# Kernel tuning notes

Measured on AMD Instinct MI355X. Metric: run time of the kernel, lower is better.

Reference implementation:

```python
import jax, jax.numpy as jnp
import numpy as np

D = 512
H = 8
W = 128  # window_size
HD = D // H
EPS = 1e-5


def _layernorm(x, g, b):
    mu = jnp.mean(x, axis=-1, keepdims=True)
    var = jnp.mean(jnp.square(x - mu), axis=-1, keepdims=True)
    return (x - mu) * jax.lax.rsqrt(var + EPS) * g + b


def setup_inputs() -> dict:
    key = jax.random.key(0)
    ks = jax.random.split(key, 6)
    B, S = 4, 8192
    src = jax.random.normal(ks[0], (B, S, D), jnp.float32)
    sc = 1.0 / np.sqrt(D)
    in_proj_w = jax.random.normal(ks[1], (3 * D, D), jnp.float32) * sc
    in_proj_b = jnp.zeros((3 * D,), jnp.float32)
    out_w = jax.random.normal(ks[2], (D, D), jnp.float32) * sc
    out_b = jnp.zeros((D,), jnp.float32)
    w1 = jax.random.normal(ks[3], (4 * D, D), jnp.float32) * sc
    b1 = jnp.zeros((4 * D,), jnp.float32)
    w2 = jax.random.normal(ks[4], (D, 4 * D), jnp.float32) * (1.0 / np.sqrt(4 * D))
    b2 = jnp.zeros((D,), jnp.float32)
    return {
        'src': src,
        'in_proj_w': in_proj_w, 'in_proj_b': in_proj_b,
        'out_w': out_w, 'out_b': out_b,
        'ln1_g': jnp.ones((D,), jnp.float32), 'ln1_b': jnp.zeros((D,), jnp.float32),
        'w1': w1, 'b1': b1, 'w2': w2, 'b2': b2,
        'ln2_g': jnp.ones((D,), jnp.float32), 'ln2_b': jnp.zeros((D,), jnp.float32),
    }


def reference(src, in_proj_w, in_proj_b, out_w, out_b, ln1_g, ln1_b,
              w1, b1, w2, b2, ln2_g, ln2_b):
    B, S, _ = src.shape
    nW = S // W
    x = src.reshape(B, nW, W, D)  # block-diagonal windows
    # packed qkv projection (torch MultiheadAttention in_proj)
    qkv = jnp.einsum('bnwd,ed->bnwe', x, in_proj_w) + in_proj_b
    q, k, v = jnp.split(qkv, 3, axis=-1)
    q = q.reshape(B, nW, W, H, HD)
    k = k.reshape(B, nW, W, H, HD)
    v = v.reshape(B, nW, W, H, HD)
    scores = jnp.einsum('bnqhd,bnkhd->bnhqk', q, k) / np.sqrt(HD)
    probs = jax.nn.softmax(scores, axis=-1)
    attn = jnp.einsum('bnhqk,bnkhd->bnqhd', probs, v).reshape(B, nW, W, D)
    attn = jnp.einsum('bnwd,ed->bnwe', attn, out_w) + out_b
    x = _layernorm(x + attn, ln1_g, ln1_b)
    ff = jnp.einsum('bnwf,df->bnwd', jax.nn.relu(jnp.einsum('bnwd,fd->bnwf', x, w1) + b1), w2) + b2
    x = _layernorm(x + ff, ln2_g, ln2_b)
    return x.reshape(B, S, D)
```

## Files before the change

### kernel.cpp

```cpp
#include <hip/hip_runtime.h>
#include <hip/hip_bf16.h>
#include <math.h>

typedef __bf16 bf16;
typedef bf16 bf16x8 __attribute__((ext_vector_type(8)));
typedef bf16 bf16x4 __attribute__((ext_vector_type(4)));
typedef float f32x4 __attribute__((ext_vector_type(4)));

#define MFMA16(a, b, c) __builtin_amdgcn_mfma_f32_16x16x32_bf16(a, b, c, 0, 0, 0)

__device__ __forceinline__ uint32_t swz(uint32_t base, uint32_t row, uint32_t rs, uint32_t cb) {
    return base + row * rs + (((cb >> 4) ^ (row & 7u)) << 4) + (cb & 15u);
}

__device__ __forceinline__ void gload16(const void* g, void* l) {
    __builtin_amdgcn_global_load_lds((const __attribute__((address_space(1))) void*)g,
                                     (__attribute__((address_space(3))) void*)l, 16, 0, 0);
}



__global__ void wcvt_kernel(const float* __restrict__ wqkv, const float* __restrict__ wout,
                            const float* __restrict__ w1f, const float* __restrict__ w2f,
                            bf16* __restrict__ o) {
    int i = blockIdx.x * blockDim.x + threadIdx.x;
    const float* s;
    int soff, doff;
    if (i < 98304) {
        int u = i;
        int tile = u >> 10, c = (u >> 8) & 3, nn = u & 255;
        int n = (tile >> 4) * 256 + nn;
        int k = (tile & 15) * 32 + c * 8;
        s = wqkv; soff = n * 512 + k; doff = u * 8;
    } else if (i < 131072) {
        int u = i - 98304;
        int tile = u >> 11, c = (u >> 9) & 3, nn = u & 511;
        int k = tile * 32 + c * 8;
        s = wout; soff = nn * 512 + k; doff = 786432 + u * 8;
    } else if (i < 262144) {
        int u = i - 131072;
        int tile = u >> 10, c = (u >> 8) & 3, nn = u & 255;
        int n = (tile >> 4) * 256 + nn;
        int k = (tile & 15) * 32 + c * 8;
        s = w1f; soff = n * 512 + k; doff = 1048576 + u * 8;
    } else {
        int u = i - 262144;
        int t = u >> 11, c = (u >> 9) & 3, nn = u & 511;
        int k = t * 32 + c * 8;
        s = w2f; soff = nn * 2048 + k; doff = 2097152 + u * 8;
    }
    float4 v0 = *(const float4*)(s + soff);
    float4 v1 = *(const float4*)(s + soff + 4);
    bf16x8 h = { (bf16)v0.x, (bf16)v0.y, (bf16)v0.z, (bf16)v0.w,
                 (bf16)v1.x, (bf16)v1.y, (bf16)v1.z, (bf16)v1.w };
    *(bf16x8*)(o + doff) = h;
}

__global__ void xcvt_kernel(float* __restrict__ src) {
    int row = blockIdx.x * 4 + (threadIdx.x >> 6);
    int l = threadIdx.x & 63;
    float* rp = src + (size_t)row * 512 + l * 8;
    float4 v0 = *(const float4*)rp;
    float4 v1 = *(const float4*)(rp + 4);
    asm volatile("s_waitcnt vmcnt(0)" ::: "memory");
    bf16x8 h = { (bf16)v0.x, (bf16)v0.y, (bf16)v0.z, (bf16)v0.w,
                 (bf16)v1.x, (bf16)v1.y, (bf16)v1.z, (bf16)v1.w };
    *(bf16x8*)((bf16*)(src + (size_t)row * 512) + l * 8) = h;
}

#define N256_LOOP(NT)                                                                  \
    int ib = 0;                                                                        \
    _Pragma("unroll 1")                                                                \
    for (int t = 0; t < (NT); ++t) {                                                   \
        int in2 = ib + 2; if (in2 >= 3) in2 -= 3;                                      \
        const uint32_t A0 = (uint32_t)ib * 8192u;                                      \
        const uint32_t B0 = 24576u + (uint32_t)ib * 16384u;                            \
        bf16x8 a[4], b[4];                                                             \
        _Pragma("unroll")                                                              \
        for (int i = 0; i < 4; ++i)                                                    \
            a[i] = *(const bf16x8*)(smem + A0 + quad * 2048 + (wm * 64 + i * 16 + l16) * 16); \
        _Pragma("unroll")                                                              \
        for (int nt = 0; nt < 4; ++nt)                                                 \
            b[nt] = *(const bf16x8*)(smem + B0 + quad * 4096 + (wn * 64 + nt * 16 + l16) * 16); \
        if (t + 2 < (NT)) { STAGE_A(in2, t + 2); STAGE_B2(in2, t + 2, 0); STAGE_B2(in2, t + 2, 1); } \
        _Pragma("unroll")                                                              \
        for (int nt = 0; nt < 4; ++nt)                                                 \
            _Pragma("unroll")                                                          \
            for (int i = 0; i < 4; ++i) acc[i][nt] = MFMA16(a[i], b[nt], acc[i][nt]);  \
        if (t + 2 < (NT)) asm volatile("s_waitcnt vmcnt(3)" ::: "memory");             \
        else              asm volatile("s_waitcnt vmcnt(0)" ::: "memory");             \
        __builtin_amdgcn_s_barrier();                                                  \
        ib = (ib == 2) ? 0 : ib + 1;                                                   \
    }

#define PHASED_LOOP(NT)                                                                \
    int ib = 0;                                                                        \
    _Pragma("unroll 1")                                                                \
    for (int t = 0; t < (NT); ++t) {                                                   \
        int in2 = ib + 2; if (in2 >= 3) in2 -= 3;                                      \
        const uint32_t A0 = (uint32_t)ib * 8192u;                                      \
        const uint32_t B0 = 24576u + (uint32_t)ib * 32768u;                            \
        bf16x8 a[4], b[8];                                                             \
                                                                \
        _Pragma("unroll")                                                              \
        for (int i = 0; i < 4; ++i)                                                    \
            a[i] = *(const bf16x8*)(smem + A0 + quad * 2048 + (wm * 64 + i * 16 + l16) * 16); \
        _Pragma("unroll")                                                              \
        for (int nt = 0; nt < 4; ++nt)                                                 \
            b[nt] = *(const bf16x8*)(smem + B0 + quad * 8192 + (wn * 128 + nt * 16 + l16) * 16); \
        if (t + 2 < (NT)) { STAGE_A(in2, t + 2); STAGE_B(in2, t + 2, 0); }             \
        __builtin_amdgcn_s_barrier();                                                  \
        asm volatile("s_waitcnt lgkmcnt(0)" ::: "memory");                             \
        __builtin_amdgcn_sched_barrier(0);                                             \
        __builtin_amdgcn_s_setprio(1);                                                 \
        _Pragma("unroll")                                                              \
        for (int nt = 0; nt < 4; ++nt)                                                 \
            _Pragma("unroll")                                                          \
            for (int i = 0; i < 4; ++i) acc[i][nt] = MFMA16(a[i], b[nt], acc[i][nt]);  \
        __builtin_amdgcn_s_setprio(0);                                                 \
        __builtin_amdgcn_s_barrier();                                                  \
                                                                \
        _Pragma("unroll")                                                              \
        for (int nt = 4; nt < 8; ++nt)                                                 \
            b[nt] = *(const bf16x8*)(smem + B0 + quad * 8192 + (wn * 128 + nt * 16 + l16) * 16); \
        if (t + 2 < (NT)) { STAGE_B(in2, t + 2, 1); STAGE_B(in2, t + 2, 2); STAGE_B(in2, t + 2, 3); } \
        __builtin_amdgcn_s_barrier();                                                  \
        asm volatile("s_waitcnt lgkmcnt(0)" ::: "memory");                             \
        __builtin_amdgcn_sched_barrier(0);                                             \
        __builtin_amdgcn_s_setprio(1);                                                 \
        _Pragma("unroll")                                                              \
        for (int nt = 4; nt < 8; ++nt)                                                 \
            _Pragma("unroll")                                                          \
            for (int i = 0; i < 4; ++i) acc[i][nt] = MFMA16(a[i], b[nt], acc[i][nt]);  \
        __builtin_amdgcn_s_setprio(0);                                                 \
        if (t + 2 < (NT)) asm volatile("s_waitcnt vmcnt(5)" ::: "memory");             \
        else              asm volatile("s_waitcnt vmcnt(0)" ::: "memory");             \
        __builtin_amdgcn_s_barrier();                                                  \
        ib = (ib == 2) ? 0 : ib + 1;                                                   \
    }

extern "C" __global__ __launch_bounds__(512, 4)
void qkv_kernel(const char* __restrict__ xb, const char* __restrict__ Wqkvp,
                const float* __restrict__ bqkv, char* __restrict__ qOb,
                char* __restrict__ kvb) {
    extern __shared__ char smem[];
    const int tid = threadIdx.x;
    const int w = tid >> 6, lane = tid & 63, l16 = lane & 15, quad = lane >> 4;
    const int wm = w >> 2, wn = w & 3;
    const int mb = blockIdx.x, cb = blockIdx.y;

    f32x4 acc[4][4];
#pragma unroll
    for (int i = 0; i < 4; ++i)
#pragma unroll
        for (int nt = 0; nt < 4; ++nt) acc[i][nt] = (f32x4){0.f, 0.f, 0.f, 0.f};

#define STAGE_A(ib_, t_)                                                               \
    {                                                                                  \
        int ca = w >> 1, rg = w & 1;                                                   \
        gload16(xb + (size_t)(mb * 128 + rg * 64 + lane) * 2048 + (t_) * 64 + ca * 16, \
                smem + (uint32_t)(ib_) * 8192u + ca * 2048 + rg * 1024);               \
    }
#define STAGE_B2(ib_, t_, j_)                                                          \
    {                                                                                  \
        int idx = w * 2 + (j_), c = idx >> 2, ng = idx & 3;                            \
        gload16(Wqkvp + (size_t)(cb * 16 + (t_)) * 16384 + c * 4096 + ng * 1024 + lane * 16, \
                smem + 24576u + (uint32_t)(ib_) * 16384u + (uint32_t)c * 4096 + (uint32_t)ng * 1024); \
    }

    STAGE_A(0, 0); STAGE_B2(0, 0, 0); STAGE_B2(0, 0, 1);
    STAGE_A(1, 1); STAGE_B2(1, 1, 0); STAGE_B2(1, 1, 1);
    asm volatile("s_waitcnt vmcnt(3)" ::: "memory");
    __builtin_amdgcn_s_barrier();

    N256_LOOP(16)
#undef STAGE_A
#undef STAGE_B2

    const uint32_t sb = 24576u + (uint32_t)w * 2048u;
#pragma unroll
    for (int i = 0; i < 4; ++i) {
#pragma unroll
        for (int nt = 0; nt < 4; ++nt) {
            float bb = bqkv[cb * 256 + wn * 64 + nt * 16 + l16];
#pragma unroll
            for (int r = 0; r < 4; ++r)
                *(bf16*)(smem + swz(sb, quad * 4 + r, 128, (nt * 16 + l16) * 2)) =
                    (bf16)(acc[i][nt][r] + bb);
        }
        asm volatile("s_waitcnt lgkmcnt(0)" ::: "memory");
#pragma unroll
        for (int t2 = 0; t2 < 2; ++t2) {
            int row = t2 * 8 + (lane >> 3), ch = lane & 7;
            bf16x8 v = *(bf16x8*)(smem + swz(sb, row, 128, ch * 16));
            size_t row_g = (size_t)(mb * 128 + wm * 64 + i * 16 + row);
            int cbyte = wn * 128 + ch * 16;
            if (cb < 2)      *(bf16x8*)(qOb + row_g * 1024 + cb * 512 + cbyte) = v;
            else if (cb < 4) *(bf16x8*)(kvb + row_g * 2048 + (cb - 2) * 512 + cbyte) = v;
            else             *(bf16x8*)(kvb + row_g * 2048 + 1024 + (cb - 4) * 512 + cbyte) = v;
        }
        asm volatile("s_waitcnt lgkmcnt(0)" ::: "memory");
    }
}

#define AVT 0u
#define ASCR 16384u
extern "C" __global__ __launch_bounds__(512, 4)
void attn_kernel(char* __restrict__ qOb, const char* __restrict__ kvb) {
    extern __shared__ char smem[];
    const int tid = threadIdx.x;
    const int wid = tid >> 6, lane = tid & 63, l16 = lane & 15, quad = lane >> 4;
    const int win = blockIdx.x >> 3, head = blockIdx.x & 7;
    const size_t wrow0 = (size_t)win * 128;
    f32x4 zero4 = { 0.f, 0.f, 0.f, 0.f };

    {
        int key = tid >> 2, d0 = (tid & 3) * 16;
        const char* vs = kvb + (wrow0 + key) * 2048 + 1024 + head * 128 + d0 * 2;
#pragma unroll
        for (int j = 0; j < 2; ++j) {
            bf16x8 v = *(const bf16x8*)(vs + j * 16);
#pragma unroll
            for (int e = 0; e < 8; ++e)
                *(bf16*)(smem + swz(AVT, d0 + j * 8 + e, 256, key * 2)) = v[e];
        }
    }
    __syncthreads();

    bf16x8 qf[2];
#pragma unroll
    for (int ks = 0; ks < 2; ++ks)
        qf[ks] = *(const bf16x8*)(qOb + (wrow0 + wid * 16 + l16) * 1024 + head * 128 + ks * 64 + quad * 16);

    f32x4 sa[8];
#pragma unroll
    for (int nt = 0; nt < 8; ++nt) sa[nt] = zero4;
#pragma unroll
    for (int nt = 0; nt < 8; ++nt)
#pragma unroll
        for (int ks = 0; ks < 2; ++ks) {
            bf16x8 kb = *(const bf16x8*)(kvb + (wrow0 + nt * 16 + l16) * 2048 + head * 128 + ks * 64 + quad * 16);
            sa[nt] = MFMA16(qf[ks], kb, sa[nt]);
        }
#pragma unroll
    for (int nt = 0; nt < 8; ++nt) sa[nt] *= 0.125f;
#pragma unroll
    for (int r = 0; r < 4; ++r) {
        float m = sa[0][r];
#pragma unroll
        for (int nt = 1; nt < 8; ++nt) m = fmaxf(m, sa[nt][r]);
#pragma unroll
        for (int sft = 1; sft < 16; sft <<= 1) m = fmaxf(m, __shfl_xor(m, sft, 64));
        float s = 0.f;
#pragma unroll
        for (int nt = 0; nt < 8; ++nt) {
            float e = __expf(sa[nt][r] - m);
            sa[nt][r] = e;
            s += e;
        }
#pragma unroll
        for (int sft = 1; sft < 16; sft <<= 1) s += __shfl_xor(s, sft, 64);
        float inv = 1.0f / s;
#pragma unroll
        for (int nt = 0; nt < 8; ++nt) sa[nt][r] *= inv;
    }

    const uint32_t sb = ASCR + (uint32_t)wid * 2048;
    bf16x8 pf[4];
#pragma unroll
    for (int hf = 0; hf < 2; ++hf) {
#pragma unroll
        for (int nt = 0; nt < 4; ++nt)
#pragma unroll
            for (int r = 0; r < 4; ++r)
                *(bf16*)(smem + swz(sb, quad * 4 + r, 128, (nt * 16 + l16) * 2)) = (bf16)sa[hf * 4 + nt][r];
        asm volatile("s_waitcnt lgkmcnt(0)" ::: "memory");
#pragma unroll
        for (int ks = 0; ks < 2; ++ks)
            pf[hf * 2 + ks] = *(bf16x8*)(smem + swz(sb, l16, 128, ks * 64 + quad * 16));
        asm volatile("s_waitcnt lgkmcnt(0)" ::: "memory");
    }

    f32x4 ov[4];
#pragma unroll
    for (int nt = 0; nt < 4; ++nt) {
        ov[nt] = zero4;
#pragma unroll
        for (int ks = 0; ks < 4; ++ks) {
            bf16x8 vb = *(bf16x8*)(smem + swz(AVT, nt * 16 + l16, 256, ks * 64 + quad * 16));
            ov[nt] = MFMA16(pf[ks], vb, ov[nt]);
        }
    }
#pragma unroll
    for (int hf = 0; hf < 2; ++hf) {
#pragma unroll
        for (int nt = 0; nt < 2; ++nt)
#pragma unroll
            for (int r = 0; r < 4; ++r)
                *(bf16*)(smem + swz(sb, quad * 4 + r, 128, (nt * 16 + l16) * 2)) = (bf16)ov[hf * 2 + nt][r];
        asm volatile("s_waitcnt lgkmcnt(0)" ::: "memory");
        {
            int row = lane >> 2, ch = lane & 3;
            bf16x8 v = *(bf16x8*)(smem + swz(sb, row, 128, ch * 16));
            *(bf16x8*)(qOb + (wrow0 + wid * 16 + row) * 1024 + head * 128 + hf * 64 + ch * 16) = v;
        }
        asm volatile("s_waitcnt lgkmcnt(0)" ::: "memory");
    }
}

extern "C" __global__ __launch_bounds__(512, 2)
void outproj_kernel(char* __restrict__ srcb, const char* __restrict__ qOb,
                    const char* __restrict__ Woutp, const float* __restrict__ bout,
                    const float* __restrict__ g1, const float* __restrict__ be1) {
    extern __shared__ char smem[];
    const int tid = threadIdx.x;
    const int w = tid >> 6, lane = tid & 63, l16 = lane & 15, quad = lane >> 4;
    const int wm = w >> 2, wn = w & 3;
    const int mb = blockIdx.x;

    f32x4 acc[4][8];
#pragma unroll
    for (int i = 0; i < 4; ++i)
#pragma unroll
        for (int nt = 0; nt < 8; ++nt) acc[i][nt] = (f32x4){0.f, 0.f, 0.f, 0.f};

#define STAGE_A(ib_, t_)                                                               \
    {                                                                                  \
        int ca = w >> 1, rg = w & 1;                                                   \
        gload16(qOb + (size_t)(mb * 128 + rg * 64 + lane) * 1024 + (t_) * 64 + ca * 16, \
                smem + (uint32_t)(ib_) * 8192u + ca * 2048 + rg * 1024);               \
    }
#define STAGE_B(ib_, t_, j_)                                                           \
    {                                                                                  \
        int idx = w * 4 + (j_), c = idx >> 3, ng = idx & 7;                            \
        gload16(Woutp + (size_t)(t_) * 32768 + c * 8192 + ng * 1024 + lane * 16,       \
                smem + 24576u + (uint32_t)(ib_) * 32768u + (uint32_t)c * 8192 + (uint32_t)ng * 1024); \
    }

    STAGE_A(0, 0); STAGE_B(0, 0, 0); STAGE_B(0, 0, 1); STAGE_B(0, 0, 2); STAGE_B(0, 0, 3);
    STAGE_A(1, 1); STAGE_B(1, 1, 0); STAGE_B(1, 1, 1); STAGE_B(1, 1, 2); STAGE_B(1, 1, 3);
    asm volatile("s_waitcnt vmcnt(5)" ::: "memory");
    __builtin_amdgcn_s_barrier();

    PHASED_LOOP(16)
#undef STAGE_A
#undef STAGE_B

#pragma unroll
    for (int nt = 0; nt < 8; ++nt) {
        int col = wn * 128 + nt * 16 + l16;
        float bb = bout[col];
#pragma unroll
        for (int i = 0; i < 4; ++i)
#pragma unroll
            for (int r = 0; r < 4; ++r) {
                int row = mb * 128 + wm * 64 + i * 16 + quad * 4 + r;
                float xv = (float)*(const bf16*)(srcb + (size_t)row * 2048 + col * 2);
                acc[i][nt][r] += bb + xv;
            }
    }
    float ps[4][4], ps2[4][4];
#pragma unroll
    for (int i = 0; i < 4; ++i)
#pragma unroll
        for (int r = 0; r < 4; ++r) {
            float s = 0.f, s2 = 0.f;
#pragma unroll
            for (int nt = 0; nt < 8; ++nt) {
                float v = acc[i][nt][r];
                s += v;
                s2 += v * v;
            }
#pragma unroll
            for (int sft = 1; sft < 16; sft <<= 1) {
                s += __shfl_xor(s, sft, 64);
                s2 += __shfl_xor(s2, sft, 64);
            }
            ps[i][r] = s;
            ps2[i][r] = s2;
        }
    if (l16 == 0) {
#pragma unroll
        for (int i = 0; i < 4; ++i)
#pragma unroll
            for (int r = 0; r < 4; ++r) {
                int row_l = wm * 64 + i * 16 + quad * 4 + r;
                *(float*)(smem + row_l * 32 + wn * 8) = ps[i][r];
                *(float*)(smem + row_l * 32 + wn * 8 + 4) = ps2[i][r];
            }
    }
    __syncthreads();
    const uint32_t sb = 24576u + (uint32_t)w * 4096u;
#pragma unroll
    for (int i = 0; i < 4; ++i) {
#pragma unroll
        for (int r = 0; r < 4; ++r) {
            int row_l = wm * 64 + i * 16 + quad * 4 + r;
            float S = 0.f, S2 = 0.f;
#pragma unroll
            for (int w4 = 0; w4 < 4; ++w4) {
                S += *(const float*)(smem + row_l * 32 + w4 * 8);
                S2 += *(const float*)(smem + row_l * 32 + w4 * 8 + 4);
            }
            float mu = S * (1.0f / 512.0f);
            float var = S2 * (1.0f / 512.0f) - mu * mu;
            float rstd = rsqrtf(var + 1e-5f);
#pragma unroll
            for (int nt = 0; nt < 8; ++nt) {
                int col = wn * 128 + nt * 16 + l16;
                float v = (acc[i][nt][r] - mu) * rstd * g1[col] + be1[col];
                *(bf16*)(smem + swz(sb, quad * 4 + r, 256, (nt * 16 + l16) * 2)) = (bf16)v;
            }
        }
        asm volatile("s_waitcnt lgkmcnt(0)" ::: "memory");
#pragma unroll
        for (int j = 0; j < 4; ++j) {
            int uu = j * 64 + lane;
            int row = uu >> 4, ch = uu & 15;
            bf16x8 v = *(bf16x8*)(smem + swz(sb, row, 256, ch * 16));
            *(bf16x8*)(srcb + (size_t)(mb * 128 + wm * 64 + i * 16 + row) * 2048 + 1024 +
                       wn * 256 + ch * 16) = v;
        }
        asm volatile("s_waitcnt lgkmcnt(0)" ::: "memory");
    }
}

extern "C" __global__ __launch_bounds__(512, 4)
void ff1_kernel(char* __restrict__ srcb, const char* __restrict__ W1p,
                const float* __restrict__ b1, char* __restrict__ doutb,
                char* __restrict__ wsOb) {
    extern __shared__ char smem[];
    const int tid = threadIdx.x;
    const int w = tid >> 6, lane = tid & 63, l16 = lane & 15, quad = lane >> 4;
    const int wm = w >> 2, wn = w & 3;
    const int mb = blockIdx.x, cb = blockIdx.y;

    f32x4 acc[4][4];
#pragma unroll
    for (int i = 0; i < 4; ++i)
#pragma unroll
        for (int nt = 0; nt < 4; ++nt) acc[i][nt] = (f32x4){0.f, 0.f, 0.f, 0.f};

#define STAGE_A(ib_, t_)                                                               \
    {                                                                                  \
        int ca = w >> 1, rg = w & 1;                                                   \
        gload16(srcb + (size_t)(mb * 128 + rg * 64 + lane) * 2048 + 1024 + (t_) * 64 + ca * 16, \
                smem + (uint32_t)(ib_) * 8192u + ca * 2048 + rg * 1024);               \
    }
#define STAGE_B2(ib_, t_, j_)                                                          \
    {                                                                                  \
        int idx = w * 2 + (j_), c = idx >> 2, ng = idx & 3;                            \
        gload16(W1p + (size_t)(cb * 16 + (t_)) * 16384 + c * 4096 + ng * 1024 + lane * 16, \
                smem + 24576u + (uint32_t)(ib_) * 16384u + (uint32_t)c * 4096 + (uint32_t)ng * 1024); \
    }

    STAGE_A(0, 0); STAGE_B2(0, 0, 0); STAGE_B2(0, 0, 1);
    STAGE_A(1, 1); STAGE_B2(1, 1, 0); STAGE_B2(1, 1, 1);
    asm volatile("s_waitcnt vmcnt(3)" ::: "memory");
    __builtin_amdgcn_s_barrier();

    N256_LOOP(16)
#undef STAGE_A
#undef STAGE_B2

    const uint32_t sb = 24576u + (uint32_t)w * 2048u;
#pragma unroll
    for (int i = 0; i < 4; ++i) {
#pragma unroll
        for (int nt = 0; nt < 4; ++nt) {
            float bb = b1[cb * 256 + wn * 64 + nt * 16 + l16];
#pragma unroll
            for (int r = 0; r < 4; ++r)
                *(bf16*)(smem + swz(sb, quad * 4 + r, 128, (nt * 16 + l16) * 2)) =
                    (bf16)fmaxf(acc[i][nt][r] + bb, 0.0f);
        }
        asm volatile("s_waitcnt lgkmcnt(0)" ::: "memory");
#pragma unroll
        for (int t2 = 0; t2 < 2; ++t2) {
            int row = t2 * 8 + (lane >> 3), ch = lane & 7;
            bf16x8 v = *(bf16x8*)(smem + swz(sb, row, 128, ch * 16));
            size_t row_g = (size_t)(mb * 128 + wm * 64 + i * 16 + row);
            int cbyte = wn * 128 + ch * 16;
            if (cb < 4)      *(bf16x8*)(doutb + row_g * 2048 + cb * 512 + cbyte) = v;
            else if (cb < 6) *(bf16x8*)(srcb + row_g * 2048 + (cb - 4) * 512 + cbyte) = v;
            else             *(bf16x8*)(wsOb + row_g * 1024 + (cb - 6) * 512 + cbyte) = v;
        }
        asm volatile("s_waitcnt lgkmcnt(0)" ::: "memory");
    }
}

extern "C" __global__ __launch_bounds__(512, 2)
void ff2_kernel(char* __restrict__ doutb, const char* __restrict__ srcb,
                const char* __restrict__ wsOb, const char* __restrict__ W2p,
                const float* __restrict__ b2, const float* __restrict__ g2,
                const float* __restrict__ be2) {
    extern __shared__ char smem[];
    const int tid = threadIdx.x;
    const int w = tid >> 6, lane = tid & 63, l16 = lane & 15, quad = lane >> 4;
    const int wm = w >> 2, wn = w & 3;
    const int mb = blockIdx.x;

    f32x4 acc[4][8];
#pragma unroll
    for (int i = 0; i < 4; ++i)
#pragma unroll
        for (int nt = 0; nt < 8; ++nt) acc[i][nt] = (f32x4){0.f, 0.f, 0.f, 0.f};

#define STAGE_A(ib_, t_)                                                               \
    {                                                                                  \
        const char* hb; int rstride, koffb;                                            \
        if ((t_) < 32)      { hb = doutb; rstride = 2048; koffb = (t_) * 64; }         \
        else if ((t_) < 48) { hb = srcb;  rstride = 2048; koffb = ((t_) - 32) * 64; }  \
        else                { hb = wsOb;  rstride = 1024; koffb = ((t_) - 48) * 64; }  \
        int ca = w >> 1, rg = w & 1;                                                   \
        gload16(hb + (size_t)(mb * 128 + rg * 64 + lane) * rstride + koffb + ca * 16,  \
                smem + (uint32_t)(ib_) * 8192u + ca * 2048 + rg * 1024);               \
    }
#define STAGE_B(ib_, t_, j_)                                                           \
    {                                                                                  \
        int idx = w * 4 + (j_), c = idx >> 3, ng = idx & 7;                            \
        gload16(W2p + (size_t)(t_) * 32768 + c * 8192 + ng * 1024 + lane * 16,         \
                smem + 24576u + (uint32_t)(ib_) * 32768u + (uint32_t)c * 8192 + (uint32_t)ng * 1024); \
    }

    STAGE_A(0, 0); STAGE_B(0, 0, 0); STAGE_B(0, 0, 1); STAGE_B(0, 0, 2); STAGE_B(0, 0, 3);
    STAGE_A(1, 1); STAGE_B(1, 1, 0); STAGE_B(1, 1, 1); STAGE_B(1, 1, 2); STAGE_B(1, 1, 3);
    asm volatile("s_waitcnt vmcnt(5)" ::: "memory");
    __builtin_amdgcn_s_barrier();

    PHASED_LOOP(64)
#undef STAGE_A
#undef STAGE_B

#pragma unroll
    for (int nt = 0; nt < 8; ++nt) {
        int col = wn * 128 + nt * 16 + l16;
        float bb = b2[col];
#pragma unroll
        for (int i = 0; i < 4; ++i)
#pragma unroll
            for (int r = 0; r < 4; ++r) {
                int row = mb * 128 + wm * 64 + i * 16 + quad * 4 + r;
                float x1v = (float)*(const bf16*)(srcb + (size_t)row * 2048 + 1024 + col * 2);
                acc[i][nt][r] += bb + x1v;
            }
    }
    float ps[4][4], ps2[4][4];
#pragma unroll
    for (int i = 0; i < 4; ++i)
#pragma unroll
        for (int r = 0; r < 4; ++r) {
            float s = 0.f, s2 = 0.f;
#pragma unroll
            for (int nt = 0; nt < 8; ++nt) {
                float v = acc[i][nt][r];
                s += v;
                s2 += v * v;
            }
#pragma unroll
            for (int sft = 1; sft < 16; sft <<= 1) {
                s += __shfl_xor(s, sft, 64);
                s2 += __shfl_xor(s2, sft, 64);
            }
            ps[i][r] = s;
            ps2[i][r] = s2;
        }
    if (l16 == 0) {
#pragma unroll
        for (int i = 0; i < 4; ++i)
#pragma unroll
            for (int r = 0; r < 4; ++r) {
                int row_l = wm * 64 + i * 16 + quad * 4 + r;
                *(float*)(smem + row_l * 32 + wn * 8) = ps[i][r];
                *(float*)(smem + row_l * 32 + wn * 8 + 4) = ps2[i][r];
            }
    }
    __syncthreads();
#pragma unroll
    for (int i = 0; i < 4; ++i)
#pragma unroll
        for (int r = 0; r < 4; ++r) {
            int row_l = wm * 64 + i * 16 + quad * 4 + r;
            float S = 0.f, S2 = 0.f;
#pragma unroll
            for (int w4 = 0; w4 < 4; ++w4) {
                S += *(const float*)(smem + row_l * 32 + w4 * 8);
                S2 += *(const float*)(smem + row_l * 32 + w4 * 8 + 4);
            }
            float mu = S * (1.0f / 512.0f);
            float var = S2 * (1.0f / 512.0f) - mu * mu;
            float rstd = rsqrtf(var + 1e-5f);
            size_t row = (size_t)(mb * 128 + row_l);
#pragma unroll
            for (int nt = 0; nt < 8; ++nt) {
                int col = wn * 128 + nt * 16 + l16;
                *(float*)(doutb + row * 2048 + col * 4) =
                    (acc[i][nt][r] - mu) * rstd * g2[col] + be2[col];
            }
        }
}

extern "C" void kernel_launch(void* const* d_in, const int* in_sizes, int n_in,
                              void* d_out, int out_size, void* d_ws, size_t ws_size,
                              hipStream_t stream) {
    (void)in_sizes; (void)n_in; (void)out_size; (void)ws_size;
    float* src = (float*)d_in[0];
    const float* ipw = (const float*)d_in[1];
    const float* ipb = (const float*)d_in[2];
    const float* ow  = (const float*)d_in[3];
    const float* ob  = (const float*)d_in[4];
    const float* g1  = (const float*)d_in[5];
    const float* be1 = (const float*)d_in[6];
    const float* w1  = (const float*)d_in[7];
    const float* b1  = (const float*)d_in[8];
    const float* w2  = (const float*)d_in[9];
    const float* b2  = (const float*)d_in[10];
    const float* g2  = (const float*)d_in[11];
    const float* be2 = (const float*)d_in[12];
    bf16* ws = (bf16*)d_ws;
    char* srcb = (char*)src;
    char* doutb = (char*)d_out;
    char* qOb = (char*)d_ws + 6291456;

    wcvt_kernel<<<1536, 256, 0, stream>>>(ipw, ow, w1, w2, ws);
    xcvt_kernel<<<8192, 256, 0, stream>>>(src);

    hipFuncSetAttribute((const void*)qkv_kernel, hipFuncAttributeMaxDynamicSharedMemorySize, 73728);
    hipFuncSetAttribute((const void*)attn_kernel, hipFuncAttributeMaxDynamicSharedMemorySize, 32768);
    hipFuncSetAttribute((const void*)outproj_kernel, hipFuncAttributeMaxDynamicSharedMemorySize, 122880);
    hipFuncSetAttribute((const void*)ff1_kernel, hipFuncAttributeMaxDynamicSharedMemorySize, 73728);
    hipFuncSetAttribute((const void*)ff2_kernel, hipFuncAttributeMaxDynamicSharedMemorySize, 122880);

    qkv_kernel<<<dim3(256, 6), 512, 73728, stream>>>(srcb, (const char*)ws, ipb, qOb, doutb);
    attn_kernel<<<2048, 512, 32768, stream>>>(qOb, doutb);
    outproj_kernel<<<256, 512, 122880, stream>>>(srcb, qOb, (const char*)(ws + 786432), ob, g1, be1);
    ff1_kernel<<<dim3(256, 8), 512, 73728, stream>>>(srcb, (const char*)(ws + 1048576), b1, doutb, qOb);
    ff2_kernel<<<256, 512, 122880, stream>>>(doutb, srcb, qOb, (const char*)(ws + 2097152), b2, g2, be2);
}
```

Measured before the change: 490.1 us.

## Split FF2 GEMM over two column blocks and move LayerNorm2 to separate kernel

The FF2 GEMM is now split into two 256-column halves (grid 256x2) so twice as many blocks run. Each block uses a smaller accumulator and LDS footprint, and the launch bound allows higher occupancy. The W2 packing is reordered to match the new tiling. Because each block no longer sees a full row, LayerNorm2 moves into a new ln2_kernel that reads the fp32 pre-norm output back and normalizes it in place. This adds a full extra read and write of the output in exchange for better GPU fill in the GEMM.

```diff
diff --git a/kernel.cpp b/kernel.cpp
--- a/kernel.cpp
+++ b/kernel.cpp
@@ -45,9 +45,10 @@
         s = w1f; soff = n * 512 + k; doff = 1048576 + u * 8;
     } else {
         int u = i - 262144;
-        int t = u >> 11, c = (u >> 9) & 3, nn = u & 511;
-        int k = t * 32 + c * 8;
-        s = w2f; soff = nn * 2048 + k; doff = 2097152 + u * 8;
+        int tile = u >> 10, c = (u >> 8) & 3, nn = u & 255;
+        int n = (tile >> 6) * 256 + nn;
+        int k = (tile & 63) * 32 + c * 8;
+        s = w2f; soff = n * 2048 + k; doff = 2097152 + u * 8;
     }
     float4 v0 = *(const float4*)(s + soff);
     float4 v1 = *(const float4*)(s + soff + 4);
@@ -489,22 +490,21 @@
     }
 }
 
-extern "C" __global__ __launch_bounds__(512, 2)
+extern "C" __global__ __launch_bounds__(512, 4)
 void ff2_kernel(char* __restrict__ doutb, const char* __restrict__ srcb,
                 const char* __restrict__ wsOb, const char* __restrict__ W2p,
-                const float* __restrict__ b2, const float* __restrict__ g2,
-                const float* __restrict__ be2) {
+                const float* __restrict__ b2) {
     extern __shared__ char smem[];
     const int tid = threadIdx.x;
     const int w = tid >> 6, lane = tid & 63, l16 = lane & 15, quad = lane >> 4;
     const int wm = w >> 2, wn = w & 3;
-    const int mb = blockIdx.x;
-
-    f32x4 acc[4][8];
+    const int mb = blockIdx.x, cb = blockIdx.y;
+
+    f32x4 acc[4][4];
 #pragma unroll
     for (int i = 0; i < 4; ++i)
 #pragma unroll
-        for (int nt = 0; nt < 8; ++nt) acc[i][nt] = (f32x4){0.f, 0.f, 0.f, 0.f};
+        for (int nt = 0; nt < 4; ++nt) acc[i][nt] = (f32x4){0.f, 0.f, 0.f, 0.f};
 
 #define STAGE_A(ib_, t_)                                                               \
     {                                                                                  \
@@ -516,25 +516,25 @@
         gload16(hb + (size_t)(mb * 128 + rg * 64 + lane) * rstride + koffb + ca * 16,  \
                 smem + (uint32_t)(ib_) * 8192u + ca * 2048 + rg * 1024);               \
     }
-#define STAGE_B(ib_, t_, j_)                                                           \
-    {                                                                                  \
-        int idx = w * 4 + (j_), c = idx >> 3, ng = idx & 7;                            \
-        gload16(W2p + (size_t)(t_) * 32768 + c * 8192 + ng * 1024 + lane * 16,         \
-                smem + 24576u + (uint32_t)(ib_) * 32768u + (uint32_t)c * 8192 + (uint32_t)ng * 1024); \
-    }
-
-    STAGE_A(0, 0); STAGE_B(0, 0, 0); STAGE_B(0, 0, 1); STAGE_B(0, 0, 2); STAGE_B(0, 0, 3);
-    STAGE_A(1, 1); STAGE_B(1, 1, 0); STAGE_B(1, 1, 1); STAGE_B(1, 1, 2); STAGE_B(1, 1, 3);
-    asm volatile("s_waitcnt vmcnt(5)" ::: "memory");
+#define STAGE_B2(ib_, t_, j_)                                                          \
+    {                                                                                  \
+        int idx = w * 2 + (j_), c = idx >> 2, ng = idx & 3;                            \
+        gload16(W2p + (size_t)(cb * 64 + (t_)) * 16384 + c * 4096 + ng * 1024 + lane * 16, \
+                smem + 24576u + (uint32_t)(ib_) * 16384u + (uint32_t)c * 4096 + (uint32_t)ng * 1024); \
+    }
+
+    STAGE_A(0, 0); STAGE_B2(0, 0, 0); STAGE_B2(0, 0, 1);
+    STAGE_A(1, 1); STAGE_B2(1, 1, 0); STAGE_B2(1, 1, 1);
+    asm volatile("s_waitcnt vmcnt(3)" ::: "memory");
     __builtin_amdgcn_s_barrier();
 
-    PHASED_LOOP(64)
+    N256_LOOP(64)
 #undef STAGE_A
-#undef STAGE_B
-
-#pragma unroll
-    for (int nt = 0; nt < 8; ++nt) {
-        int col = wn * 128 + nt * 16 + l16;
+#undef STAGE_B2
+
+#pragma unroll
+    for (int nt = 0; nt < 4; ++nt) {
+        int col = cb * 256 + wn * 64 + nt * 16 + l16;
         float bb = b2[col];
 #pragma unroll
         for (int i = 0; i < 4; ++i)
@@ -542,62 +542,43 @@
             for (int r = 0; r < 4; ++r) {
                 int row = mb * 128 + wm * 64 + i * 16 + quad * 4 + r;
                 float x1v = (float)*(const bf16*)(srcb + (size_t)row * 2048 + 1024 + col * 2);
-                acc[i][nt][r] += bb + x1v;
+                *(float*)(doutb + (size_t)row * 2048 + col * 4) = acc[i][nt][r] + bb + x1v;
             }
     }
-    float ps[4][4], ps2[4][4];
-#pragma unroll
-    for (int i = 0; i < 4; ++i)
-#pragma unroll
-        for (int r = 0; r < 4; ++r) {
-            float s = 0.f, s2 = 0.f;
-#pragma unroll
-            for (int nt = 0; nt < 8; ++nt) {
-                float v = acc[i][nt][r];
-                s += v;
-                s2 += v * v;
-            }
-#pragma unroll
-            for (int sft = 1; sft < 16; sft <<= 1) {
-                s += __shfl_xor(s, sft, 64);
-                s2 += __shfl_xor(s2, sft, 64);
-            }
-            ps[i][r] = s;
-            ps2[i][r] = s2;
-        }
-    if (l16 == 0) {
-#pragma unroll
-        for (int i = 0; i < 4; ++i)
-#pragma unroll
-            for (int r = 0; r < 4; ++r) {
-                int row_l = wm * 64 + i * 16 + quad * 4 + r;
-                *(float*)(smem + row_l * 32 + wn * 8) = ps[i][r];
-                *(float*)(smem + row_l * 32 + wn * 8 + 4) = ps2[i][r];
-            }
-    }
-    __syncthreads();
-#pragma unroll
-    for (int i = 0; i < 4; ++i)
-#pragma unroll
-        for (int r = 0; r < 4; ++r) {
-            int row_l = wm * 64 + i * 16 + quad * 4 + r;
-            float S = 0.f, S2 = 0.f;
-#pragma unroll
-            for (int w4 = 0; w4 < 4; ++w4) {
-                S += *(const float*)(smem + row_l * 32 + w4 * 8);
-                S2 += *(const float*)(smem + row_l * 32 + w4 * 8 + 4);
-            }
-            float mu = S * (1.0f / 512.0f);
-            float var = S2 * (1.0f / 512.0f) - mu * mu;
-            float rstd = rsqrtf(var + 1e-5f);
-            size_t row = (size_t)(mb * 128 + row_l);
-#pragma unroll
-            for (int nt = 0; nt < 8; ++nt) {
-                int col = wn * 128 + nt * 16 + l16;
-                *(float*)(doutb + row * 2048 + col * 4) =
-                    (acc[i][nt][r] - mu) * rstd * g2[col] + be2[col];
-            }
-        }
+}
+
+extern "C" __global__ __launch_bounds__(256)
+void ln2_kernel(float* __restrict__ y, const float* __restrict__ g2,
+                const float* __restrict__ be2) {
+    int row = blockIdx.x * 4 + (threadIdx.x >> 6);
+    int lane = threadIdx.x & 63;
+    float* rp = y + (size_t)row * 512 + lane * 8;
+    float4 v0 = *(const float4*)rp;
+    float4 v1 = *(const float4*)(rp + 4);
+    float s = v0.x + v0.y + v0.z + v0.w + v1.x + v1.y + v1.z + v1.w;
+    float s2 = v0.x * v0.x + v0.y * v0.y + v0.z * v0.z + v0.w * v0.w +
+               v1.x * v1.x + v1.y * v1.y + v1.z * v1.z + v1.w * v1.w;
+#pragma unroll
+    for (int sft = 1; sft < 64; sft <<= 1) {
+        s += __shfl_xor(s, sft, 64);
+        s2 += __shfl_xor(s2, sft, 64);
+    }
+    float mu = s * (1.0f / 512.0f);
+    float var = s2 * (1.0f / 512.0f) - mu * mu;
+    float rstd = rsqrtf(var + 1e-5f);
+    const float* gp = g2 + lane * 8;
+    const float* bp = be2 + lane * 8;
+    float4 o0, o1;
+    o0.x = (v0.x - mu) * rstd * gp[0] + bp[0];
+    o0.y = (v0.y - mu) * rstd * gp[1] + bp[1];
+    o0.z = (v0.z - mu) * rstd * gp[2] + bp[2];
+    o0.w = (v0.w - mu) * rstd * gp[3] + bp[3];
+    o1.x = (v1.x - mu) * rstd * gp[4] + bp[4];
+    o1.y = (v1.y - mu) * rstd * gp[5] + bp[5];
+    o1.z = (v1.z - mu) * rstd * gp[6] + bp[6];
+    o1.w = (v1.w - mu) * rstd * gp[7] + bp[7];
+    *(float4*)rp = o0;
+    *(float4*)(rp + 4) = o1;
 }
 
 extern "C" void kernel_launch(void* const* d_in, const int* in_sizes, int n_in,
@@ -629,11 +610,12 @@
     hipFuncSetAttribute((const void*)attn_kernel, hipFuncAttributeMaxDynamicSharedMemorySize, 32768);
     hipFuncSetAttribute((const void*)outproj_kernel, hipFuncAttributeMaxDynamicSharedMemorySize, 122880);
     hipFuncSetAttribute((const void*)ff1_kernel, hipFuncAttributeMaxDynamicSharedMemorySize, 73728);
-    hipFuncSetAttribute((const void*)ff2_kernel, hipFuncAttributeMaxDynamicSharedMemorySize, 122880);
+    hipFuncSetAttribute((const void*)ff2_kernel, hipFuncAttributeMaxDynamicSharedMemorySize, 73728);
 
     qkv_kernel<<<dim3(256, 6), 512, 73728, stream>>>(srcb, (const char*)ws, ipb, qOb, doutb);
     attn_kernel<<<2048, 512, 32768, stream>>>(qOb, doutb);
     outproj_kernel<<<256, 512, 122880, stream>>>(srcb, qOb, (const char*)(ws + 786432), ob, g1, be1);
     ff1_kernel<<<dim3(256, 8), 512, 73728, stream>>>(srcb, (const char*)(ws + 1048576), b1, doutb, qOb);
-    ff2_kernel<<<256, 512, 122880, stream>>>(doutb, srcb, qOb, (const char*)(ws + 2097152), b2, g2, be2);
-}
+    ff2_kernel<<<dim3(256, 2), 512, 73728, stream>>>(doutb, srcb, qOb, (const char*)(ws + 2097152), b2);
+    ln2_kernel<<<8192, 256, 0, stream>>>((float*)doutb, g2, be2);
+}
```

Result: no change. 488.6 us (-0.3%).
